# Performance work log

Hardware: AMD Instinct MI355X
Metric: run time of the kernel (lower is better)

## Reference

```python
import jax, jax.numpy as jnp
import numpy as np
from jax import lax

DIM = 180
NH = 6
WS = (16, 16)          # window_size
BWS = (8, 8)           # base_win_size (min of base and window)
HEAD_DIM = DIM // (2 * NH)      # 15
SCALE = HEAD_DIM
POS_DIM = (DIM // 4) // 4       # 11 (DynamicPosBias pos_dim on dim//4)
B, H, W = 2, 256, 256
L = WS[0] * WS[1]               # 256 tokens per window
ML = BWS[0] * BWS[1]            # 64 downsampled tokens
R = L // ML                     # 4, spatial_linear in_features


def _rel_index():
    Hs, Ws = WS
    coords = np.stack(np.meshgrid(np.arange(Hs), np.arange(Ws), indexing='ij')).reshape(2, -1)
    rel = (coords[:, :, None] - coords[:, None, :]).transpose(1, 2, 0)
    rel[..., 0] += Hs - 1
    rel[..., 1] += Ws - 1
    rel[..., 0] *= 2 * Ws - 1
    return jnp.asarray(rel.sum(-1).reshape(-1))  # (L*L,) indices into (2H-1)*(2W-1)


def _bias_grid():
    Hs, Ws = WS
    g = np.stack(np.meshgrid(np.arange(1 - Hs, Hs), np.arange(1 - Ws, Ws), indexing='ij'))
    return jnp.asarray(g.reshape(2, -1).T.astype(np.float32))  # ((2H-1)*(2W-1), 2)

REL_IDX = _rel_index()
BIAS_GRID = _bias_grid()


def _ln(x, g, b):
    m = x.mean(-1, keepdims=True)
    v = ((x - m) ** 2).mean(-1, keepdims=True)
    return (x - m) / jnp.sqrt(v + 1e-5) * g + b


def window_partition(x, ws):
    Bn, Hn, Wn, C = x.shape
    x = x.reshape(Bn, Hn // ws[0], ws[0], Wn // ws[1], ws[1], C)
    return x.transpose(0, 1, 3, 2, 4, 5).reshape(-1, ws[0], ws[1], C)


def window_reverse(w, ws, Hn, Wn):
    Bn = w.shape[0] * (ws[0] * ws[1]) // (Hn * Wn)
    x = w.reshape(Bn, Hn // ws[0], Wn // ws[1], ws[0], ws[1], -1)
    return x.transpose(0, 1, 3, 2, 4, 5).reshape(Bn, Hn, Wn, -1)


def setup_inputs():
    key = jax.random.key(0)
    ks = jax.random.split(key, 16)
    s = 0.02
    rn = lambda k, shape: jax.random.normal(k, shape, jnp.float32) * s
    C5 = DIM // 5
    return {
        'x': jax.random.normal(ks[0], (B, H, W, DIM), jnp.float32),
        'conv1_w': rn(ks[1], (DIM, C5)), 'conv1_b': jnp.zeros((C5,), jnp.float32),
        'conv2_w': rn(ks[2], (3, 3, C5, C5)), 'conv2_b': jnp.zeros((C5,), jnp.float32),
        'conv3_w': rn(ks[3], (C5, DIM)), 'conv3_b': jnp.zeros((DIM,), jnp.float32),
        'dfe_lin_w': rn(ks[4], (DIM, DIM)), 'dfe_lin_b': jnp.zeros((DIM,), jnp.float32),
        'sl_w': rn(ks[5], (R,)), 'sl_b': jnp.zeros((), jnp.float32),
        'pos_proj_w': rn(ks[6], (2, POS_DIM)), 'pos_proj_b': jnp.zeros((POS_DIM,), jnp.float32),
        'ln1_g': jnp.ones((POS_DIM,), jnp.float32), 'ln1_b': jnp.zeros((POS_DIM,), jnp.float32),
        'mlp1_w': rn(ks[7], (POS_DIM, POS_DIM)), 'mlp1_b': jnp.zeros((POS_DIM,), jnp.float32),
        'ln2_g': jnp.ones((POS_DIM,), jnp.float32), 'ln2_b': jnp.zeros((POS_DIM,), jnp.float32),
        'mlp2_w': rn(ks[8], (POS_DIM, POS_DIM)), 'mlp2_b': jnp.zeros((POS_DIM,), jnp.float32),
        'ln3_g': jnp.ones((POS_DIM,), jnp.float32), 'ln3_b': jnp.zeros((POS_DIM,), jnp.float32),
        'mlp3_w': rn(ks[9], (POS_DIM, NH)), 'mlp3_b': jnp.zeros((NH,), jnp.float32),
        'proj_w': rn(ks[10], (DIM, DIM)), 'proj_b': jnp.zeros((DIM,), jnp.float32),
    }


def reference(x, conv1_w, conv1_b, conv2_w, conv2_b, conv3_w, conv3_b,
              dfe_lin_w, dfe_lin_b, sl_w, sl_b, pos_proj_w, pos_proj_b,
              ln1_g, ln1_b, mlp1_w, mlp1_b, ln2_g, ln2_b, mlp2_w, mlp2_b,
              ln3_g, ln3_b, mlp3_w, mlp3_b, proj_w, proj_b):
    xB, xH, xW, xC = x.shape

    # ---- DFE: qv = conv(x) * linear(x), both in NHWC ----
    y = jax.nn.leaky_relu(x @ conv1_w + conv1_b, 0.2)
    y = lax.conv_general_dilated(y, conv2_w, (1, 1), 'SAME',
                                 dimension_numbers=('NHWC', 'HWIO', 'NHWC'))
    y = jax.nn.leaky_relu(y + conv2_b, 0.2)
    y = y @ conv3_w + conv3_b
    qv = y * (x @ dfe_lin_w + dfe_lin_b)            # (B,H,W,C)

    # ---- window partition + q/v head split ----
    qv = window_partition(qv, WS).reshape(-1, L, xC)       # (Bw,L,C)
    Bw = qv.shape[0]
    qv = qv.reshape(Bw, L, 2, NH, HEAD_DIM).transpose(2, 0, 3, 1, 4)
    q, v = qv[0], qv[1]                                    # (Bw,NH,L,hd)

    # ---- spatial self-correlation ----
    mH, mW = BWS
    rH, rW = WS[0] // mH, WS[1] // mW
    v_ = v.reshape(Bw, NH, mH, rH, mW, rW, HEAD_DIM)
    v_ = v_.transpose(0, 1, 2, 4, 6, 3, 5).reshape(Bw, NH, ML, HEAD_DIM, rH * rW)
    vp = jnp.einsum('bhmcr,r->bhmc', v_, sl_w) + sl_b      # (Bw,NH,ML,hd)

    corr = jnp.einsum('bhlc,bhmc->bhlm', q, vp) / SCALE    # (Bw,NH,L,ML)

    # dynamic relative position bias MLP (residual=False)
    p = BIAS_GRID @ pos_proj_w + pos_proj_b
    p = jax.nn.relu(_ln(p, ln1_g, ln1_b)) @ mlp1_w + mlp1_b
    p = jax.nn.relu(_ln(p, ln2_g, ln2_b)) @ mlp2_w + mlp2_b
    p = jax.nn.relu(_ln(p, ln3_g, ln3_b)) @ mlp3_w + mlp3_b  # ((2H-1)*(2W-1), NH)

    rpb = p[REL_IDX].reshape(L, mH, rH, mW, rW, NH)
    rpb = rpb.transpose(0, 1, 3, 5, 2, 4).reshape(L, ML, NH, rH * rW).mean(-1)
    rpb = rpb.transpose(2, 0, 1)                            # (NH,L,ML)
    corr = corr + rpb[None]

    x_sp = jnp.einsum('bhlm,bhmc->bhlc', corr, vp)
    x_sp = x_sp.transpose(0, 2, 1, 3).reshape(Bw, L, NH * HEAD_DIM)

    # ---- channel self-correlation ----
    qc = q.transpose(0, 2, 1, 3).reshape(Bw, L, NH * HEAD_DIM)
    vc = v.transpose(0, 2, 1, 3).reshape(Bw, L, NH * HEAD_DIM)
    cc = jnp.einsum('blc,bld->bcd', qc, vc) / L
    x_ch = jnp.einsum('bcd,bld->blc', cc, vc)

    # ---- merge windows, concat, project ----
    half = xC // 2
    x_sp = window_reverse(x_sp.reshape(-1, WS[0], WS[1], half), WS, xH, xW)
    x_ch = window_reverse(x_ch.reshape(-1, WS[0], WS[1], half), WS, xH, xW)
    out = jnp.concatenate([x_sp, x_ch], -1) @ proj_w + proj_b
    return out
```

## Files before the change

kernel.cpp:

```cpp
#include <hip/hip_runtime.h>
#include <hip/hip_fp16.h>

typedef unsigned int uint32;
typedef _Float16 f16;
typedef f16 f16x4 __attribute__((ext_vector_type(4)));
typedef f16 f16x8 __attribute__((ext_vector_type(8)));
typedef float f32x4 __attribute__((ext_vector_type(4)));

union U8 { f16x8 v; uint4 u4; uint2 u2[2]; f16 h[8]; };

__device__ __forceinline__ float h2f(__half v) { return __half2float(v); }
__device__ __forceinline__ __half f2h(float v) { return __float2half(v); }

__global__ __launch_bounds__(256) void k0_w1(const float* __restrict__ W1,
                                             f16* __restrict__ W1T) {
  int i = blockIdx.x * 256 + threadIdx.x;
  if (i < 9216) {
    int n = i / 192, k = i % 192;
    W1T[i] = (n < 36 && k < 180) ? (f16)W1[k * 36 + n] : (f16)0;
  }
}

__global__ __launch_bounds__(256) void k1_conv1(const float* __restrict__ X,
                                                const f16* __restrict__ W1T,
                                                const float* __restrict__ B1,
                                                __half* __restrict__ T1) {
  int t = threadIdx.x;
  int p0 = blockIdx.x * 128;
  int lane = t & 63, wave = t >> 6;
  int lm = lane & 15, lq = lane >> 4;

  f16x8 ax[6][2];
#pragma unroll
  for (int mt = 0; mt < 2; ++mt) {
    int row = p0 + wave * 32 + mt * 16 + lm;
    const float* xr = X + (size_t)row * 180;
#pragma unroll
    for (int ch = 0; ch < 6; ++ch) {
      int k0 = ch * 32 + lq * 8;
      U8 v; v.u4 = (uint4){0u, 0u, 0u, 0u};
      if (k0 + 8 <= 180) {
        float4 a = *(const float4*)&xr[k0];
        float4 b = *(const float4*)&xr[k0 + 4];
        v.h[0]=(f16)a.x; v.h[1]=(f16)a.y; v.h[2]=(f16)a.z; v.h[3]=(f16)a.w;
        v.h[4]=(f16)b.x; v.h[5]=(f16)b.y; v.h[6]=(f16)b.z; v.h[7]=(f16)b.w;
      } else if (k0 < 180) {
        float4 a = *(const float4*)&xr[k0];
        v.h[0]=(f16)a.x; v.h[1]=(f16)a.y; v.h[2]=(f16)a.z; v.h[3]=(f16)a.w;
      }
      ax[ch][mt] = v.v;
    }
  }

  f32x4 acc[2][3];
#pragma unroll
  for (int mt = 0; mt < 2; ++mt)
#pragma unroll
    for (int nt = 0; nt < 3; ++nt) acc[mt][nt] = (f32x4){0.f, 0.f, 0.f, 0.f};

#pragma unroll
  for (int ch = 0; ch < 6; ++ch) {
#pragma unroll
    for (int nt = 0; nt < 3; ++nt) {
      int n = nt * 16 + lm;
      f16x8 bf = *(const f16x8*)&W1T[n * 192 + ch * 32 + lq * 8];
      acc[0][nt] = __builtin_amdgcn_mfma_f32_16x16x32_f16(
          ax[ch][0], bf, acc[0][nt], 0, 0, 0);
      acc[1][nt] = __builtin_amdgcn_mfma_f32_16x16x32_f16(
          ax[ch][1], bf, acc[1][nt], 0, 0, 0);
    }
  }

  float bb[3];
#pragma unroll
  for (int nt = 0; nt < 3; ++nt) {
    int co = nt * 16 + lm;
    bb[nt] = (co < 36) ? B1[co] : 0.f;
  }
#pragma unroll
  for (int mt = 0; mt < 2; ++mt) {
#pragma unroll
    for (int reg = 0; reg < 4; ++reg) {
      int p = p0 + wave * 32 + mt * 16 + lq * 4 + reg;
      __half* o = T1 + (size_t)p * 36;
#pragma unroll
      for (int nt = 0; nt < 3; ++nt) {
        int co = nt * 16 + lm;
        if (co < 36) {
          float v = acc[mt][nt][reg] + bb[nt];
          o[co] = f2h(v > 0.f ? v : 0.2f * v);
        }
      }
    }
  }
}

__global__ __launch_bounds__(256) void k0_w2(const float* __restrict__ W2,
                                             f16* __restrict__ W2T) {
  int i = blockIdx.x * 256 + threadIdx.x;
  if (i < 17280) {
    int tap = i / 1920, rem = i % 1920, n = rem / 40, k = rem % 40;
    W2T[i] = (n < 36 && k < 36) ? (f16)W2[(tap * 36 + k) * 36 + n] : (f16)0;
  }
}

__global__ __launch_bounds__(256) void k2_conv2(const __half* __restrict__ T1,
                                                const f16* __restrict__ W2T,
                                                const float* __restrict__ B2,
                                                __half* __restrict__ T2) {
  __shared__ __align__(16) f16 ins[3 * 132 * 40];
  int t = threadIdx.x;
  int p0 = blockIdx.x * 128;
  int b = p0 >> 16, y = (p0 >> 8) & 255, x0 = p0 & 255;

  const uint32* T1u = (const uint32*)T1;
  uint32* insu = (uint32*)ins;
  for (int i = t; i < 7920; i += 256) {
    int kh = i / 2640, rem = i % 2640;
    int xx = rem / 20, u = rem % 20;
    int ry = y + kh - 1, gx = x0 + xx - 1;
    uint32 v = 0u;
    if (u < 18 && xx < 130 && (unsigned)ry < 256u && (unsigned)gx < 256u)
      v = T1u[((size_t)((b * 256 + ry) * 256 + gx)) * 18 + u];
    insu[i] = v;
  }
  __syncthreads();

  int lane = t & 63, wave = t >> 6;
  int lm = lane & 15, lq = lane >> 4;
  const f16x8 zero8 = {(f16)0,(f16)0,(f16)0,(f16)0,(f16)0,(f16)0,(f16)0,(f16)0};

  f32x4 acc[2][3];
#pragma unroll
  for (int mt = 0; mt < 2; ++mt)
#pragma unroll
    for (int nt = 0; nt < 3; ++nt) acc[mt][nt] = (f32x4){0.f, 0.f, 0.f, 0.f};

#pragma unroll
  for (int kh = 0; kh < 3; ++kh) {
#pragma unroll
    for (int kw = 0; kw < 3; ++kw) {
      int tap = kh * 3 + kw;
      f16x8 a0[2], a1[2];
#pragma unroll
      for (int mt = 0; mt < 2; ++mt) {
        int xx = wave * 32 + mt * 16 + lm + kw;
        const f16* ar = &ins[(kh * 132 + xx) * 40];
        a0[mt] = *(const f16x8*)&ar[lq * 8];
        a1[mt] = (lq == 0) ? *(const f16x8*)&ar[32] : zero8;
      }
#pragma unroll
      for (int nt = 0; nt < 3; ++nt) {
        const f16* br = &W2T[(tap * 48 + nt * 16 + lm) * 40];
        f16x8 b0 = *(const f16x8*)&br[lq * 8];
        f16x8 b1 = (lq == 0) ? *(const f16x8*)&br[32] : zero8;
#pragma unroll
        for (int mt = 0; mt < 2; ++mt) {
          acc[mt][nt] = __builtin_amdgcn_mfma_f32_16x16x32_f16(
              a0[mt], b0, acc[mt][nt], 0, 0, 0);
          acc[mt][nt] = __builtin_amdgcn_mfma_f32_16x16x32_f16(
              a1[mt], b1, acc[mt][nt], 0, 0, 0);
        }
      }
    }
  }

  float bb[3];
#pragma unroll
  for (int nt = 0; nt < 3; ++nt) {
    int co = nt * 16 + lm;
    bb[nt] = (co < 36) ? B2[co] : 0.f;
  }
#pragma unroll
  for (int mt = 0; mt < 2; ++mt) {
#pragma unroll
    for (int reg = 0; reg < 4; ++reg) {
      int p = p0 + wave * 32 + mt * 16 + lq * 4 + reg;
      __half* o = T2 + (size_t)p * 36;
#pragma unroll
      for (int nt = 0; nt < 3; ++nt) {
        int co = nt * 16 + lm;
        if (co < 36) {
          float v = acc[mt][nt][reg] + bb[nt];
          o[co] = f2h(v > 0.f ? v : 0.2f * v);
        }
      }
    }
  }
}

__global__ __launch_bounds__(256) void k0_wt(const float* __restrict__ SW3,
                                             const float* __restrict__ SWD,
                                             f16* __restrict__ WT3,
                                             f16* __restrict__ WTD) {
  int tid = blockIdx.x * 256 + threadIdx.x;
  int stride = gridDim.x * 256;
  for (int i = tid; i < 192 * 40; i += stride) {
    int n = i / 40, k = i % 40;
    WT3[i] = (n < 180 && k < 36) ? (f16)SW3[k * 180 + n] : (f16)0;
  }
  for (int i = tid; i < 192 * 192; i += stride) {
    int n = i / 192, k = i % 192;
    WTD[i] = (n < 180 && k < 180) ? (f16)SWD[k * 180 + n] : (f16)0;
  }
}

__global__ __launch_bounds__(256) void k0_pw(const float* __restrict__ SPW,
                                             f16* __restrict__ PWT) {
  int tid = blockIdx.x * 256 + threadIdx.x;
  int stride = gridDim.x * 256;
  for (int i = tid; i < 192 * 192; i += stride) {
    int n = i / 192, k = i % 192;
    PWT[i] = (n < 180 && k < 180) ? (f16)SPW[k * 180 + n] : (f16)0;
  }
}

__global__ __launch_bounds__(256) void k3_qv(const float* __restrict__ X,
                                             const __half* __restrict__ T2,
                                             const f16* __restrict__ WT3,
                                             const f16* __restrict__ WTD,
                                             const float* __restrict__ B3,
                                             const float* __restrict__ BD,
                                             __half* __restrict__ QX) {
  __shared__ __align__(16) f16 eplds[4 * 32 * 56];
  int t = threadIdx.x;
  int p0 = blockIdx.x * 128;
  int lane = t & 63, wave = t >> 6;
  int lm = lane & 15, lq = lane >> 4;

  const f16x8 zero8 = {(f16)0,(f16)0,(f16)0,(f16)0,(f16)0,(f16)0,(f16)0,(f16)0};

  f16x8 ax[6][2];
  f16x8 at0[2];
  f16x8 at1[2];
#pragma unroll
  for (int mt = 0; mt < 2; ++mt) {
    int row = p0 + wave * 32 + mt * 16 + lm;
    const float* xr = X + (size_t)row * 180;
#pragma unroll
    for (int ch = 0; ch < 6; ++ch) {
      int k0 = ch * 32 + lq * 8;
      U8 v; v.u4 = (uint4){0u, 0u, 0u, 0u};
      if (k0 + 8 <= 180) {
        float4 a = *(const float4*)&xr[k0];
        float4 b = *(const float4*)&xr[k0 + 4];
        v.h[0]=(f16)a.x; v.h[1]=(f16)a.y; v.h[2]=(f16)a.z; v.h[3]=(f16)a.w;
        v.h[4]=(f16)b.x; v.h[5]=(f16)b.y; v.h[6]=(f16)b.z; v.h[7]=(f16)b.w;
      } else if (k0 < 180) {
        float4 a = *(const float4*)&xr[k0];
        v.h[0]=(f16)a.x; v.h[1]=(f16)a.y; v.h[2]=(f16)a.z; v.h[3]=(f16)a.w;
      }
      ax[ch][mt] = v.v;
    }
    const f16* tr = (const f16*)T2 + (size_t)row * 36;
    U8 tv;
    tv.u2[0] = *(const uint2*)&tr[lq * 8];
    tv.u2[1] = *(const uint2*)&tr[lq * 8 + 4];
    at0[mt] = tv.v;
    U8 t1v; t1v.u4 = (uint4){0u, 0u, 0u, 0u};
    if (lq == 0) t1v.u2[0] = *(const uint2*)&tr[32];
    at1[mt] = t1v.v;
  }

  f16* myl = eplds + wave * 1792;
  for (int bn = 0; bn < 4; ++bn) {
    int n0 = bn * 48;
    f32x4 accC[2][3], accD[2][3];
#pragma unroll
    for (int i = 0; i < 2; ++i)
#pragma unroll
      for (int j = 0; j < 3; ++j) {
        accC[i][j] = (f32x4){0.f, 0.f, 0.f, 0.f};
        accD[i][j] = (f32x4){0.f, 0.f, 0.f, 0.f};
      }

#pragma unroll
    for (int nt = 0; nt < 3; ++nt) {
      int n = n0 + nt * 16 + lm;
      f16x8 b0 = *(const f16x8*)&WT3[n * 40 + lq * 8];
      f16x8 b1 = (lq == 0) ? *(const f16x8*)&WT3[n * 40 + 32] : zero8;
#pragma unroll
      for (int mt = 0; mt < 2; ++mt) {
        accC[mt][nt] = __builtin_amdgcn_mfma_f32_16x16x32_f16(
            at0[mt], b0, accC[mt][nt], 0, 0, 0);
        accC[mt][nt] = __builtin_amdgcn_mfma_f32_16x16x32_f16(
            at1[mt], b1, accC[mt][nt], 0, 0, 0);
      }
    }

#pragma unroll
    for (int ch = 0; ch < 6; ++ch) {
#pragma unroll
      for (int nt = 0; nt < 3; ++nt) {
        int n = n0 + nt * 16 + lm;
        f16x8 bf = *(const f16x8*)&WTD[n * 192 + ch * 32 + lq * 8];
        accD[0][nt] = __builtin_amdgcn_mfma_f32_16x16x32_f16(
            ax[ch][0], bf, accD[0][nt], 0, 0, 0);
        accD[1][nt] = __builtin_amdgcn_mfma_f32_16x16x32_f16(
            ax[ch][1], bf, accD[1][nt], 0, 0, 0);
      }
    }

    float cb[3], db[3];
#pragma unroll
    for (int nt = 0; nt < 3; ++nt) {
      int col = n0 + nt * 16 + lm;
      cb[nt] = (col < 180) ? B3[col] : 0.f;
      db[nt] = (col < 180) ? BD[col] : 0.f;
    }
#pragma unroll
    for (int mt = 0; mt < 2; ++mt)
#pragma unroll
      for (int reg = 0; reg < 4; ++reg) {
        int r = mt * 16 + lq * 4 + reg;
#pragma unroll
        for (int nt = 0; nt < 3; ++nt)
          myl[r * 56 + nt * 16 + lm] =
              (f16)((accC[mt][nt][reg] + cb[nt]) *
                    (accD[mt][nt][reg] + db[nt]) * 64.f);
      }
#pragma unroll
    for (int it = 0; it < 6; ++it) {
      int idx = it * 64 + lane;
      int r = idx / 12, c4 = idx % 12;
      int col = n0 + c4 * 4;
      if (col < 180) {
        int p = p0 + wave * 32 + r;
        int b = p >> 16, y = (p >> 8) & 255, x = p & 255;
        int wi = (b << 8) | ((y >> 4) << 4) | (x >> 4);
        int l = ((y & 15) << 4) | (x & 15);
        uint2 val = *(const uint2*)&myl[r * 56 + c4 * 4];
        *(uint2*)((f16*)QX + ((size_t)(wi * 256 + l)) * 180 + col) = val;
      }
    }
  }
}

__device__ __forceinline__ void ln_relu11(const float* p, const float* g,
                                          const float* b, float* r) {
  float m = 0.f;
#pragma unroll
  for (int j = 0; j < 11; ++j) m += p[j];
  m *= (1.0f / 11.0f);
  float v = 0.f;
#pragma unroll
  for (int j = 0; j < 11; ++j) { float d = p[j] - m; v += d * d; }
  v *= (1.0f / 11.0f);
  float inv = 1.0f / sqrtf(v + 1e-5f);
#pragma unroll
  for (int j = 0; j < 11; ++j) {
    float xn = (p[j] - m) * inv * g[j] + b[j];
    r[j] = fmaxf(xn, 0.f);
  }
}
__device__ __forceinline__ void mm11(const float* r, const float* W,
                                     const float* b, float* o) {
#pragma unroll
  for (int j2 = 0; j2 < 11; ++j2) {
    float s = b[j2];
#pragma unroll
    for (int j = 0; j < 11; ++j) s += r[j] * W[j * 11 + j2];
    o[j2] = s;
  }
}

__global__ __launch_bounds__(256) void k5a_posmlp(
    const float* PPW, const float* PPB,
    const float* LN1G, const float* LN1B, const float* M1W, const float* M1B,
    const float* LN2G, const float* LN2B, const float* M2W, const float* M2B,
    const float* LN3G, const float* LN3B, const float* M3W, const float* M3B,
    float* __restrict__ PTAB) {
  int t = blockIdx.x * 256 + threadIdx.x;
  if (t >= 961) return;
  float g0 = (float)(t / 31) - 15.0f;
  float g1 = (float)(t % 31) - 15.0f;
  float p[11], r[11];
#pragma unroll
  for (int j = 0; j < 11; ++j)
    p[j] = g0 * PPW[j] + g1 * PPW[11 + j] + PPB[j];
  ln_relu11(p, LN1G, LN1B, r);
  mm11(r, M1W, M1B, p);
  ln_relu11(p, LN2G, LN2B, r);
  mm11(r, M2W, M2B, p);
  ln_relu11(p, LN3G, LN3B, r);
#pragma unroll
  for (int h = 0; h < 6; ++h) {
    float s = M3B[h];
#pragma unroll
    for (int j = 0; j < 11; ++j) s += r[j] * M3W[j * 6 + h];
    PTAB[t * 6 + h] = s;
  }
}

__global__ __launch_bounds__(256) void k5b_rpb(const float* __restrict__ PTAB,
                                               float* __restrict__ RPB) {
  int t = blockIdx.x * 256 + threadIdx.x;
  int m = t & 63;
  int l = (t >> 6) & 255;
  int h = t >> 14;
  int mh = m >> 3, mw = m & 7;
  int qr = l >> 4, qc = l & 15;
  float s = 0.f;
#pragma unroll
  for (int rh = 0; rh < 2; ++rh)
#pragma unroll
    for (int rw = 0; rw < 2; ++rw) {
      int dr = qr - (mh * 2 + rh) + 15;
      int dc = qc - (mw * 2 + rw) + 15;
      s += PTAB[(dr * 31 + dc) * 6 + h];
    }
  RPB[t] = 0.25f * s;
}

__global__ __launch_bounds__(256) void k7a_cc(const __half* __restrict__ QX,
                                              float* __restrict__ CC) {
  __shared__ __half qs[64 * 90];
  __shared__ __half vs[64 * 90];
  int wi = blockIdx.x, t = threadIdx.x;
  int c0 = (t % 15) * 6, d0 = (t / 15) * 6;
  bool act = t < 225;
  float acc[36];
#pragma unroll
  for (int i = 0; i < 36; ++i) acc[i] = 0.f;
  const uint32* G = (const uint32*)(QX + (size_t)wi * 46080);
  uint32* qsw = (uint32*)qs;
  uint32* vsw = (uint32*)vs;
  for (int pass = 0; pass < 4; ++pass) {
    __syncthreads();
    for (int i = t; i < 2880; i += 256) {
      int l = i / 45, k = i % 45;
      int gw = (pass * 64 + l) * 90;
      qsw[l * 45 + k] = G[gw + k];
      vsw[l * 45 + k] = G[gw + 45 + k];
    }
    __syncthreads();
    if (act) {
      for (int l = 0; l < 64; ++l) {
        const __half2* qh = (const __half2*)&qs[l * 90 + c0];
        const __half2* vh = (const __half2*)&vs[l * 90 + d0];
        float a[6], b[6];
#pragma unroll
        for (int k = 0; k < 3; ++k) {
          __half2 x = qh[k];
          a[2 * k] = __low2float(x); a[2 * k + 1] = __high2float(x);
          __half2 y = vh[k];
          b[2 * k] = __low2float(y); b[2 * k + 1] = __high2float(y);
        }
#pragma unroll
        for (int i = 0; i < 6; ++i)
#pragma unroll
          for (int j = 0; j < 6; ++j) acc[i * 6 + j] += a[i] * b[j];
      }
    }
  }
  if (act) {
    const float s = 1.0f / (256.0f * 4096.0f);
#pragma unroll
    for (int i = 0; i < 6; ++i)
#pragma unroll
      for (int j = 0; j < 6; ++j)
        CC[((size_t)(wi * 90 + c0 + i)) * 90 + d0 + j] = acc[i * 6 + j] * s;
  }
}

__global__ __launch_bounds__(256) void kA_xsp(__half* __restrict__ QX,
                                              const float* __restrict__ RPB,
                                              const float* __restrict__ SLW,
                                              const float* __restrict__ SLB) {
  __shared__ __align__(16) unsigned char SM[80384];
  f16* U   = (f16*)SM;
  f16* vpS = (f16*)(SM + 53248);
  f16* vpT = (f16*)(SM + 66560);
  int wi = blockIdx.x, t = threadIdx.x;
  __half* QW = QX + (size_t)wi * 46080;
  const uint32* G = (const uint32*)QW;
  uint32* Uw = (uint32*)U;

  for (int i = t; i < 11520; i += 256) {
    int l = i / 45, k = i % 45;
    Uw[l * 45 + k] = G[l * 90 + 45 + k];
  }
  __syncthreads();
  float w0 = SLW[0], w1 = SLW[1], w2 = SLW[2], w3 = SLW[3];
  float sb = SLB[0];
  for (int e = t; e < 6144; e += 256) {
    int m = e & 63, idx = e >> 6;
    int c = idx & 15, h = idx >> 4;
    f16 val = (f16)0;
    if (c < 15) {
      int ch = h * 15 + c;
      int lb = (m >> 3) * 32 + (m & 7) * 2;
      float s = w0 * (float)U[lb * 90 + ch] + w1 * (float)U[(lb + 1) * 90 + ch]
              + w2 * (float)U[(lb + 16) * 90 + ch] + w3 * (float)U[(lb + 17) * 90 + ch];
      val = (f16)(s * 4.f + sb * 256.f);
    }
    vpS[m * 104 + idx] = val;
    vpT[idx * 72 + m] = val;
  }
  __syncthreads();
  for (int j = t; j < 1536; j += 256) {
    int h = j >> 8, l = j & 255;
    U[l * 104 + h * 16 + 15] = (f16)0;
  }
  for (int i = t; i < 11520; i += 256) {
    int l = i / 45, k = i % 45;
    union { uint32 w; f16 h[2]; } cv;
    cv.w = G[l * 90 + k];
    int cg0 = 2 * k, cg1 = 2 * k + 1;
    int h0 = cg0 / 15, c0 = cg0 - h0 * 15;
    int h1 = cg1 / 15, c1 = cg1 - h1 * 15;
    U[l * 104 + h0 * 16 + c0] = cv.h[0];
    U[l * 104 + h1 * 16 + c1] = cv.h[1];
  }
  __syncthreads();

  int lane = t & 63, w = t >> 6;
  int lm = lane & 15, lq = lane >> 4;
  const float invA = 1.0f / 960.0f;
  for (int h = 0; h < 6; ++h) {
    f16x4 a1[4], b1[4];
#pragma unroll
    for (int mt = 0; mt < 4; ++mt)
      a1[mt] = *(const f16x4*)&vpS[(mt * 16 + lm) * 104 + h * 16 + lq * 4];
#pragma unroll
    for (int lt = 0; lt < 4; ++lt)
      b1[lt] = *(const f16x4*)&U[(w * 64 + lt * 16 + lm) * 104 + h * 16 + lq * 4];
    f32x4 acc1[4][4];
#pragma unroll
    for (int mt = 0; mt < 4; ++mt)
#pragma unroll
      for (int lt = 0; lt < 4; ++lt)
        acc1[mt][lt] = __builtin_amdgcn_mfma_f32_16x16x16f16(
            a1[mt], b1[lt], (f32x4){0.f, 0.f, 0.f, 0.f}, 0, 0, 0);
    f16x4 b2[4][4];
#pragma unroll
    for (int lt = 0; lt < 4; ++lt) {
      int l = w * 64 + lt * 16 + lm;
      const float* rp = RPB + ((size_t)(h * 256 + l)) * 64;
#pragma unroll
      for (int mt = 0; mt < 4; ++mt) {
        float4 rv = *(const float4*)&rp[mt * 16 + lq * 4];
        f16x4 bb;
        bb[0] = (f16)(acc1[mt][lt][0] * invA + rv.x * 256.f);
        bb[1] = (f16)(acc1[mt][lt][1] * invA + rv.y * 256.f);
        bb[2] = (f16)(acc1[mt][lt][2] * invA + rv.z * 256.f);
        bb[3] = (f16)(acc1[mt][lt][3] * invA + rv.w * 256.f);
        b2[mt][lt] = bb;
      }
    }
    f16x4 a2[4];
#pragma unroll
    for (int kt = 0; kt < 4; ++kt)
      a2[kt] = *(const f16x4*)&vpT[(h * 16 + lm) * 72 + kt * 16 + lq * 4];
#pragma unroll
    for (int lt = 0; lt < 4; ++lt) {
      f32x4 acc2 = (f32x4){0.f, 0.f, 0.f, 0.f};
#pragma unroll
      for (int kt = 0; kt < 4; ++kt)
        acc2 = __builtin_amdgcn_mfma_f32_16x16x16f16(a2[kt], b2[kt][lt], acc2, 0, 0, 0);
      int l = w * 64 + lt * 16 + lm;
      __half* orow = QW + l * 180 + h * 15;
#pragma unroll
      for (int reg = 0; reg < 4; ++reg) {
        int c = lq * 4 + reg;
        if (c < 15) orow[c] = f2h(acc2[reg] * 0.125f);
      }
    }
  }
}

__global__ __launch_bounds__(256) void kB_xch(__half* __restrict__ QX,
                                              const float* __restrict__ CC) {
  __shared__ __align__(16) f16 vA[256 * 104];
  __shared__ __align__(16) f16 ccB[96 * 104];
  int wi = blockIdx.x, t = threadIdx.x;
  __half* QW = QX + (size_t)wi * 46080;
  const uint32* G = (const uint32*)QW;
  uint32* vAw = (uint32*)vA;
  for (int i = t; i < 12288; i += 256) {
    int l = i / 48, kk = i % 48;
    vAw[l * 52 + kk] = (kk < 45) ? G[l * 90 + 45 + kk] : 0u;
  }
  const float* ccg = CC + (size_t)wi * 8100;
  uint32* ccw = (uint32*)ccB;
  for (int i = t; i < 4992; i += 256) {
    int c = i / 52, dd = i % 52;
    uint32 out = 0u;
    if (c < 90 && dd < 45) {
      float2 f = *(const float2*)&ccg[c * 90 + dd * 2];
      union { uint32 w; f16 h[2]; } cv;
      cv.h[0] = (f16)(f.x * 65536.f);
      cv.h[1] = (f16)(f.y * 65536.f);
      out = cv.w;
    }
    ccw[c * 52 + dd] = out;
  }
  __syncthreads();
  int lane = t & 63, w = t >> 6;
  int lm = lane & 15, lq = lane >> 4;
  f32x4 acc[4][6];
#pragma unroll
  for (int mt = 0; mt < 4; ++mt)
#pragma unroll
    for (int nt = 0; nt < 6; ++nt) acc[mt][nt] = (f32x4){0.f, 0.f, 0.f, 0.f};
  for (int kc = 0; kc < 3; ++kc) {
    f16x8 af[4], bf[6];
#pragma unroll
    for (int mt = 0; mt < 4; ++mt)
      af[mt] = *(const f16x8*)&vA[(w * 64 + mt * 16 + lm) * 104 + kc * 32 + lq * 8];
#pragma unroll
    for (int nt = 0; nt < 6; ++nt)
      bf[nt] = *(const f16x8*)&ccB[(nt * 16 + lm) * 104 + kc * 32 + lq * 8];
#pragma unroll
    for (int mt = 0; mt < 4; ++mt)
#pragma unroll
      for (int nt = 0; nt < 6; ++nt)
        acc[mt][nt] = __builtin_amdgcn_mfma_f32_16x16x32_f16(
            af[mt], bf[nt], acc[mt][nt], 0, 0, 0);
  }
#pragma unroll
  for (int mt = 0; mt < 4; ++mt) {
#pragma unroll
    for (int reg = 0; reg < 4; ++reg) {
      int l = w * 64 + mt * 16 + lq * 4 + reg;
      __half* orow = QW + l * 180 + 90;
#pragma unroll
      for (int nt = 0; nt < 6; ++nt) {
        int c = nt * 16 + lm;
        if (c < 90) orow[c] = f2h(acc[mt][nt][reg] * 0.001953125f);
      }
    }
  }
}

__global__ __launch_bounds__(256) void k8_proj(const __half* __restrict__ XS,
                                               const f16* __restrict__ PWT,
                                               const float* __restrict__ PB,
                                               float* __restrict__ OUT) {
  int t = threadIdx.x;
  int w0r = blockIdx.x * 128;
  int lane = t & 63, wave = t >> 6;
  int lm = lane & 15, lq = lane >> 4;

  f16x8 ax[6][2];
#pragma unroll
  for (int mt = 0; mt < 2; ++mt) {
    int row = w0r + wave * 32 + mt * 16 + lm;
    const f16* xr = (const f16*)XS + (size_t)row * 180;
#pragma unroll
    for (int ch = 0; ch < 6; ++ch) {
      int k0 = ch * 32 + lq * 8;
      U8 v; v.u4 = (uint4){0u, 0u, 0u, 0u};
      if (k0 + 8 <= 180) {
        v.u2[0] = *(const uint2*)&xr[k0];
        v.u2[1] = *(const uint2*)&xr[k0 + 4];
      } else if (k0 < 180) {
        v.u2[0] = *(const uint2*)&xr[k0];
      }
      ax[ch][mt] = v.v;
    }
  }

  for (int bn = 0; bn < 4; ++bn) {
    int n0 = bn * 48;
    f32x4 acc[2][3];
#pragma unroll
    for (int i = 0; i < 2; ++i)
#pragma unroll
      for (int j = 0; j < 3; ++j) acc[i][j] = (f32x4){0.f, 0.f, 0.f, 0.f};

#pragma unroll
    for (int ch = 0; ch < 6; ++ch) {
#pragma unroll
      for (int nt = 0; nt < 3; ++nt) {
        int n = n0 + nt * 16 + lm;
        f16x8 bf = *(const f16x8*)&PWT[n * 192 + ch * 32 + lq * 8];
        acc[0][nt] = __builtin_amdgcn_mfma_f32_16x16x32_f16(
            ax[ch][0], bf, acc[0][nt], 0, 0, 0);
        acc[1][nt] = __builtin_amdgcn_mfma_f32_16x16x32_f16(
            ax[ch][1], bf, acc[1][nt], 0, 0, 0);
      }
    }

    float pb[3];
#pragma unroll
    for (int nt = 0; nt < 3; ++nt) {
      int col = n0 + nt * 16 + lm;
      pb[nt] = (col < 180) ? PB[col] : 0.f;
    }
    const float inv = 1.0f / 8192.0f;
#pragma unroll
    for (int mt = 0; mt < 2; ++mt) {
#pragma unroll
      for (int reg = 0; reg < 4; ++reg) {
        int w = w0r + wave * 32 + mt * 16 + lq * 4 + reg;
        int wi = w >> 8, l = w & 255;
        int b = wi >> 8, wy = (wi >> 4) & 15, wx = wi & 15;
        int ly = l >> 4, lx = l & 15;
        int p = (b << 16) | (((wy << 4) | ly) << 8) | ((wx << 4) | lx);
        float* orow = OUT + (size_t)p * 180;
#pragma unroll
        for (int nt = 0; nt < 3; ++nt) {
          int col = n0 + nt * 16 + lm;
          if (col < 180) orow[col] = acc[mt][nt][reg] * inv + pb[nt];
        }
      }
    }
  }
}

extern "C" void kernel_launch(void* const* d_in, const int* in_sizes, int n_in,
                              void* d_out, int out_size, void* d_ws, size_t ws_size,
                              hipStream_t stream) {
  const float* X    = (const float*)d_in[0];
  const float* W1   = (const float*)d_in[1];
  const float* B1   = (const float*)d_in[2];
  const float* W2   = (const float*)d_in[3];
  const float* B2   = (const float*)d_in[4];
  const float* W3   = (const float*)d_in[5];
  const float* B3c  = (const float*)d_in[6];
  const float* WD   = (const float*)d_in[7];
  const float* BD   = (const float*)d_in[8];
  const float* SLW  = (const float*)d_in[9];
  const float* SLB  = (const float*)d_in[10];
  const float* PPW  = (const float*)d_in[11];
  const float* PPB  = (const float*)d_in[12];
  const float* LN1G = (const float*)d_in[13];
  const float* LN1B = (const float*)d_in[14];
  const float* M1W  = (const float*)d_in[15];
  const float* M1B  = (const float*)d_in[16];
  const float* LN2G = (const float*)d_in[17];
  const float* LN2B = (const float*)d_in[18];
  const float* M2W  = (const float*)d_in[19];
  const float* M2B  = (const float*)d_in[20];
  const float* LN3G = (const float*)d_in[21];
  const float* LN3B = (const float*)d_in[22];
  const float* M3W  = (const float*)d_in[23];
  const float* M3B  = (const float*)d_in[24];
  const float* PW   = (const float*)d_in[25];
  const float* PB   = (const float*)d_in[26];
  float* OUT = (float*)d_out;

  char* ws = (char*)d_ws;
  f16*   W2T  = (f16*)(ws);
  f16*   W1T  = (f16*)(ws + 34560);
  __half* QX  = (__half*)(ws);
  __half* T1  = (__half*)(ws + 47185920);
  __half* T2  = (__half*)(ws + 56623104);
  float* PTAB = (float*)(ws + 47185920);
  float* RPB  = (float*)(ws + 47212544);
  f16*   WT3  = (f16*)(ws + 47605760);
  f16*   WTD  = (f16*)(ws + 47621120);
  float* CC   = (float*)(ws + 47605760);
  f16*   PWT  = (f16*)(ws + 64194560);

  hipLaunchKernelGGL(k0_w2, dim3(68), dim3(256), 0, stream, W2, W2T);
  hipLaunchKernelGGL(k0_w1, dim3(36), dim3(256), 0, stream, W1, W1T);
  hipLaunchKernelGGL(k1_conv1, dim3(1024), dim3(256), 0, stream, X, W1T, B1, T1);
  hipLaunchKernelGGL(k2_conv2, dim3(1024), dim3(256), 0, stream, T1, W2T, B2, T2);
  hipLaunchKernelGGL(k0_wt, dim3(144), dim3(256), 0, stream, W3, WD, WT3, WTD);
  hipLaunchKernelGGL(k3_qv, dim3(1024), dim3(256), 0, stream, X, T2, WT3, WTD, B3c, BD, QX);
  hipLaunchKernelGGL(k0_pw, dim3(144), dim3(256), 0, stream, PW, PWT);
  hipLaunchKernelGGL(k5a_posmlp, dim3(4), dim3(256), 0, stream,
                     PPW, PPB, LN1G, LN1B, M1W, M1B, LN2G, LN2B, M2W, M2B,
                     LN3G, LN3B, M3W, M3B, PTAB);
  hipLaunchKernelGGL(k5b_rpb, dim3(384), dim3(256), 0, stream, PTAB, RPB);
  hipLaunchKernelGGL(k7a_cc, dim3(512), dim3(256), 0, stream, QX, CC);
  hipLaunchKernelGGL(kA_xsp, dim3(512), dim3(256), 0, stream, QX, RPB, SLW, SLB);
  hipLaunchKernelGGL(kB_xch, dim3(512), dim3(256), 0, stream, QX, CC);
  hipLaunchKernelGGL(k8_proj, dim3(1024), dim3(256), 0, stream, QX, PWT, PB, OUT);
}
```

Baseline: 525.6 us.

## Fuse channel-correlation, spatial attention and channel output into one per-window kernel

Replaces three per-window kernels (cc computation, spatial correlation, channel output) with a single kernel that loads each window's q and v into LDS once. The channel-correlation matrix now stays in LDS as fp16 instead of making a round-trip through a global fp32 buffer, and two launches disappear. In exchange the kernel uses about 150 KB of LDS, which limits it to one block per CU. Its phases then run back to back with barriers between them, with less latency hiding.

```diff
diff --git a/kernel.cpp b/kernel.cpp
--- a/kernel.cpp
+++ b/kernel.cpp
@@ -412,32 +412,45 @@
   RPB[t] = 0.25f * s;
 }
 
-__global__ __launch_bounds__(256) void k7a_cc(const __half* __restrict__ QX,
-                                              float* __restrict__ CC) {
-  __shared__ __half qs[64 * 90];
-  __shared__ __half vs[64 * 90];
+__global__ __launch_bounds__(256) void kW_win(__half* __restrict__ QX,
+                                              const float* __restrict__ RPB,
+                                              const float* __restrict__ SLW,
+                                              const float* __restrict__ SLB) {
+  __shared__ __align__(16) unsigned char SMW[153600];
+  f16* vA  = (f16*)SMW;
+  f16* QU  = (f16*)(SMW + 53248);
+  f16* vpS = (f16*)(SMW + 106496);
+  f16* vpT = (f16*)(SMW + 119808);
+  f16* ccs = (f16*)(SMW + 133632);
   int wi = blockIdx.x, t = threadIdx.x;
-  int c0 = (t % 15) * 6, d0 = (t / 15) * 6;
-  bool act = t < 225;
-  float acc[36];
-#pragma unroll
-  for (int i = 0; i < 36; ++i) acc[i] = 0.f;
-  const uint32* G = (const uint32*)(QX + (size_t)wi * 46080);
-  uint32* qsw = (uint32*)qs;
-  uint32* vsw = (uint32*)vs;
-  for (int pass = 0; pass < 4; ++pass) {
-    __syncthreads();
-    for (int i = t; i < 2880; i += 256) {
-      int l = i / 45, k = i % 45;
-      int gw = (pass * 64 + l) * 90;
-      qsw[l * 45 + k] = G[gw + k];
-      vsw[l * 45 + k] = G[gw + 45 + k];
-    }
-    __syncthreads();
-    if (act) {
-      for (int l = 0; l < 64; ++l) {
-        const __half2* qh = (const __half2*)&qs[l * 90 + c0];
-        const __half2* vh = (const __half2*)&vs[l * 90 + d0];
+  __half* QW = QX + (size_t)wi * 46080;
+  const uint32* G = (const uint32*)QW;
+
+  uint32* vAw = (uint32*)vA;
+  for (int i = t; i < 12288; i += 256) {
+    int l = i / 48, kk = i % 48;
+    vAw[l * 52 + kk] = (kk < 45) ? G[l * 90 + 45 + kk] : 0u;
+  }
+  uint32* qlw = (uint32*)QU;
+  for (int i = t; i < 11520; i += 256) {
+    int l = i / 45, k = i % 45;
+    qlw[l * 45 + k] = G[l * 90 + k];
+  }
+  for (int i = t; i < 9984; i += 256) {
+    int c = i / 104, d = i % 104;
+    if (c >= 90 || d >= 90) ccs[i] = (f16)0;
+  }
+  __syncthreads();
+
+  {
+    int c0 = (t % 15) * 6, d0 = (t / 15) * 6;
+    if (t < 225) {
+      float acc[36];
+#pragma unroll
+      for (int i = 0; i < 36; ++i) acc[i] = 0.f;
+      for (int l = 0; l < 256; ++l) {
+        const __half2* qh = (const __half2*)&QU[l * 90 + c0];
+        const __half2* vh = (const __half2*)&vA[l * 104 + d0];
         float a[6], b[6];
 #pragma unroll
         for (int k = 0; k < 3; ++k) {
@@ -451,183 +464,139 @@
 #pragma unroll
           for (int j = 0; j < 6; ++j) acc[i * 6 + j] += a[i] * b[j];
       }
-    }
-  }
-  if (act) {
-    const float s = 1.0f / (256.0f * 4096.0f);
-#pragma unroll
-    for (int i = 0; i < 6; ++i)
-#pragma unroll
-      for (int j = 0; j < 6; ++j)
-        CC[((size_t)(wi * 90 + c0 + i)) * 90 + d0 + j] = acc[i * 6 + j] * s;
-  }
-}
-
-__global__ __launch_bounds__(256) void kA_xsp(__half* __restrict__ QX,
-                                              const float* __restrict__ RPB,
-                                              const float* __restrict__ SLW,
-                                              const float* __restrict__ SLB) {
-  __shared__ __align__(16) unsigned char SM[80384];
-  f16* U   = (f16*)SM;
-  f16* vpS = (f16*)(SM + 53248);
-  f16* vpT = (f16*)(SM + 66560);
-  int wi = blockIdx.x, t = threadIdx.x;
-  __half* QW = QX + (size_t)wi * 46080;
-  const uint32* G = (const uint32*)QW;
-  uint32* Uw = (uint32*)U;
-
-  for (int i = t; i < 11520; i += 256) {
-    int l = i / 45, k = i % 45;
-    Uw[l * 45 + k] = G[l * 90 + 45 + k];
+#pragma unroll
+      for (int i = 0; i < 6; ++i)
+#pragma unroll
+        for (int j = 0; j < 6; ++j)
+          ccs[(c0 + i) * 104 + d0 + j] = (f16)(acc[i * 6 + j] * 0.0625f);
+    }
   }
   __syncthreads();
-  float w0 = SLW[0], w1 = SLW[1], w2 = SLW[2], w3 = SLW[3];
-  float sb = SLB[0];
-  for (int e = t; e < 6144; e += 256) {
-    int m = e & 63, idx = e >> 6;
-    int c = idx & 15, h = idx >> 4;
-    f16 val = (f16)0;
-    if (c < 15) {
-      int ch = h * 15 + c;
-      int lb = (m >> 3) * 32 + (m & 7) * 2;
-      float s = w0 * (float)U[lb * 90 + ch] + w1 * (float)U[(lb + 1) * 90 + ch]
-              + w2 * (float)U[(lb + 16) * 90 + ch] + w3 * (float)U[(lb + 17) * 90 + ch];
-      val = (f16)(s * 4.f + sb * 256.f);
-    }
-    vpS[m * 104 + idx] = val;
-    vpT[idx * 72 + m] = val;
-  }
-  __syncthreads();
-  for (int j = t; j < 1536; j += 256) {
-    int h = j >> 8, l = j & 255;
-    U[l * 104 + h * 16 + 15] = (f16)0;
-  }
-  for (int i = t; i < 11520; i += 256) {
-    int l = i / 45, k = i % 45;
-    union { uint32 w; f16 h[2]; } cv;
-    cv.w = G[l * 90 + k];
-    int cg0 = 2 * k, cg1 = 2 * k + 1;
-    int h0 = cg0 / 15, c0 = cg0 - h0 * 15;
-    int h1 = cg1 / 15, c1 = cg1 - h1 * 15;
-    U[l * 104 + h0 * 16 + c0] = cv.h[0];
-    U[l * 104 + h1 * 16 + c1] = cv.h[1];
+
+  {
+    float w0 = SLW[0], w1 = SLW[1], w2 = SLW[2], w3 = SLW[3];
+    float sb = SLB[0];
+    for (int e = t; e < 6144; e += 256) {
+      int m = e & 63, idx = e >> 6;
+      int c = idx & 15, h = idx >> 4;
+      f16 val = (f16)0;
+      if (c < 15) {
+        int ch = h * 15 + c;
+        int lb = (m >> 3) * 32 + (m & 7) * 2;
+        float s = w0 * (float)vA[lb * 104 + ch] + w1 * (float)vA[(lb + 1) * 104 + ch]
+                + w2 * (float)vA[(lb + 16) * 104 + ch] + w3 * (float)vA[(lb + 17) * 104 + ch];
+        val = (f16)(s * 4.f + sb * 256.f);
+      }
+      vpS[m * 104 + idx] = val;
+      vpT[idx * 72 + m] = val;
+    }
+    for (int j = t; j < 1536; j += 256) {
+      int h = j >> 8, l = j & 255;
+      QU[l * 104 + h * 16 + 15] = (f16)0;
+    }
+    for (int i = t; i < 11520; i += 256) {
+      int l = i / 45, k = i % 45;
+      union { uint32 w; f16 h[2]; } cv;
+      cv.w = G[l * 90 + k];
+      int cg0 = 2 * k, cg1 = 2 * k + 1;
+      int h0 = cg0 / 15, c0 = cg0 - h0 * 15;
+      int h1 = cg1 / 15, c1 = cg1 - h1 * 15;
+      QU[l * 104 + h0 * 16 + c0] = cv.h[0];
+      QU[l * 104 + h1 * 16 + c1] = cv.h[1];
+    }
   }
   __syncthreads();
 
   int lane = t & 63, w = t >> 6;
   int lm = lane & 15, lq = lane >> 4;
-  const float invA = 1.0f / 960.0f;
-  for (int h = 0; h < 6; ++h) {
-    f16x4 a1[4], b1[4];
+
+  {
+    const float invA = 1.0f / 960.0f;
+    for (int h = 0; h < 6; ++h) {
+      f16x4 a1[4], b1[4];
+#pragma unroll
+      for (int mt = 0; mt < 4; ++mt)
+        a1[mt] = *(const f16x4*)&vpS[(mt * 16 + lm) * 104 + h * 16 + lq * 4];
+#pragma unroll
+      for (int lt = 0; lt < 4; ++lt)
+        b1[lt] = *(const f16x4*)&QU[(w * 64 + lt * 16 + lm) * 104 + h * 16 + lq * 4];
+      f32x4 acc1[4][4];
+#pragma unroll
+      for (int mt = 0; mt < 4; ++mt)
+#pragma unroll
+        for (int lt = 0; lt < 4; ++lt)
+          acc1[mt][lt] = __builtin_amdgcn_mfma_f32_16x16x16f16(
+              a1[mt], b1[lt], (f32x4){0.f, 0.f, 0.f, 0.f}, 0, 0, 0);
+      f16x4 b2[4][4];
+#pragma unroll
+      for (int lt = 0; lt < 4; ++lt) {
+        int l = w * 64 + lt * 16 + lm;
+        const float* rp = RPB + ((size_t)(h * 256 + l)) * 64;
+#pragma unroll
+        for (int mt = 0; mt < 4; ++mt) {
+          float4 rv = *(const float4*)&rp[mt * 16 + lq * 4];
+          f16x4 bb;
+          bb[0] = (f16)(acc1[mt][lt][0] * invA + rv.x * 256.f);
+          bb[1] = (f16)(acc1[mt][lt][1] * invA + rv.y * 256.f);
+          bb[2] = (f16)(acc1[mt][lt][2] * invA + rv.z * 256.f);
+          bb[3] = (f16)(acc1[mt][lt][3] * invA + rv.w * 256.f);
+          b2[mt][lt] = bb;
+        }
+      }
+      f16x4 a2[4];
+#pragma unroll
+      for (int kt = 0; kt < 4; ++kt)
+        a2[kt] = *(const f16x4*)&vpT[(h * 16 + lm) * 72 + kt * 16 + lq * 4];
+#pragma unroll
+      for (int lt = 0; lt < 4; ++lt) {
+        f32x4 acc2 = (f32x4){0.f, 0.f, 0.f, 0.f};
+#pragma unroll
+        for (int kt = 0; kt < 4; ++kt)
+          acc2 = __builtin_amdgcn_mfma_f32_16x16x16f16(a2[kt], b2[kt][lt], acc2, 0, 0, 0);
+        int l = w * 64 + lt * 16 + lm;
+        __half* orow = QW + l * 180 + h * 15;
+#pragma unroll
+        for (int reg = 0; reg < 4; ++reg) {
+          int c = lq * 4 + reg;
+          if (c < 15) orow[c] = f2h(acc2[reg] * 0.125f);
+        }
+      }
+    }
+  }
+  __syncthreads();
+
+  {
+    f32x4 acc[4][6];
 #pragma unroll
     for (int mt = 0; mt < 4; ++mt)
-      a1[mt] = *(const f16x4*)&vpS[(mt * 16 + lm) * 104 + h * 16 + lq * 4];
-#pragma unroll
-    for (int lt = 0; lt < 4; ++lt)
-      b1[lt] = *(const f16x4*)&U[(w * 64 + lt * 16 + lm) * 104 + h * 16 + lq * 4];
-    f32x4 acc1[4][4];
-#pragma unroll
-    for (int mt = 0; mt < 4; ++mt)
-#pragma unroll
-      for (int lt = 0; lt < 4; ++lt)
-        acc1[mt][lt] = __builtin_amdgcn_mfma_f32_16x16x16f16(
-            a1[mt], b1[lt], (f32x4){0.f, 0.f, 0.f, 0.f}, 0, 0, 0);
-    f16x4 b2[4][4];
-#pragma unroll
-    for (int lt = 0; lt < 4; ++lt) {
-      int l = w * 64 + lt * 16 + lm;
-      const float* rp = RPB + ((size_t)(h * 256 + l)) * 64;
-#pragma unroll
-      for (int mt = 0; mt < 4; ++mt) {
-        float4 rv = *(const float4*)&rp[mt * 16 + lq * 4];
-        f16x4 bb;
-        bb[0] = (f16)(acc1[mt][lt][0] * invA + rv.x * 256.f);
-        bb[1] = (f16)(acc1[mt][lt][1] * invA + rv.y * 256.f);
-        bb[2] = (f16)(acc1[mt][lt][2] * invA + rv.z * 256.f);
-        bb[3] = (f16)(acc1[mt][lt][3] * invA + rv.w * 256.f);
-        b2[mt][lt] = bb;
-      }
-    }
-    f16x4 a2[4];
-#pragma unroll
-    for (int kt = 0; kt < 4; ++kt)
-      a2[kt] = *(const f16x4*)&vpT[(h * 16 + lm) * 72 + kt * 16 + lq * 4];
-#pragma unroll
-    for (int lt = 0; lt < 4; ++lt) {
-      f32x4 acc2 = (f32x4){0.f, 0.f, 0.f, 0.f};
-#pragma unroll
-      for (int kt = 0; kt < 4; ++kt)
-        acc2 = __builtin_amdgcn_mfma_f32_16x16x16f16(a2[kt], b2[kt][lt], acc2, 0, 0, 0);
-      int l = w * 64 + lt * 16 + lm;
-      __half* orow = QW + l * 180 + h * 15;
+#pragma unroll
+      for (int nt = 0; nt < 6; ++nt) acc[mt][nt] = (f32x4){0.f, 0.f, 0.f, 0.f};
+    for (int kc = 0; kc < 3; ++kc) {
+      f16x8 af[4], bf[6];
+#pragma unroll
+      for (int mt = 0; mt < 4; ++mt)
+        af[mt] = *(const f16x8*)&vA[(w * 64 + mt * 16 + lm) * 104 + kc * 32 + lq * 8];
+#pragma unroll
+      for (int nt = 0; nt < 6; ++nt)
+        bf[nt] = *(const f16x8*)&ccs[(nt * 16 + lm) * 104 + kc * 32 + lq * 8];
+#pragma unroll
+      for (int mt = 0; mt < 4; ++mt)
+#pragma unroll
+        for (int nt = 0; nt < 6; ++nt)
+          acc[mt][nt] = __builtin_amdgcn_mfma_f32_16x16x32_f16(
+              af[mt], bf[nt], acc[mt][nt], 0, 0, 0);
+    }
+#pragma unroll
+    for (int mt = 0; mt < 4; ++mt) {
 #pragma unroll
       for (int reg = 0; reg < 4; ++reg) {
-        int c = lq * 4 + reg;
-        if (c < 15) orow[c] = f2h(acc2[reg] * 0.125f);
-      }
-    }
-  }
-}
-
-__global__ __launch_bounds__(256) void kB_xch(__half* __restrict__ QX,
-                                              const float* __restrict__ CC) {
-  __shared__ __align__(16) f16 vA[256 * 104];
-  __shared__ __align__(16) f16 ccB[96 * 104];
-  int wi = blockIdx.x, t = threadIdx.x;
-  __half* QW = QX + (size_t)wi * 46080;
-  const uint32* G = (const uint32*)QW;
-  uint32* vAw = (uint32*)vA;
-  for (int i = t; i < 12288; i += 256) {
-    int l = i / 48, kk = i % 48;
-    vAw[l * 52 + kk] = (kk < 45) ? G[l * 90 + 45 + kk] : 0u;
-  }
-  const float* ccg = CC + (size_t)wi * 8100;
-  uint32* ccw = (uint32*)ccB;
-  for (int i = t; i < 4992; i += 256) {
-    int c = i / 52, dd = i % 52;
-    uint32 out = 0u;
-    if (c < 90 && dd < 45) {
-      float2 f = *(const float2*)&ccg[c * 90 + dd * 2];
-      union { uint32 w; f16 h[2]; } cv;
-      cv.h[0] = (f16)(f.x * 65536.f);
-      cv.h[1] = (f16)(f.y * 65536.f);
-      out = cv.w;
-    }
-    ccw[c * 52 + dd] = out;
-  }
-  __syncthreads();
-  int lane = t & 63, w = t >> 6;
-  int lm = lane & 15, lq = lane >> 4;
-  f32x4 acc[4][6];
-#pragma unroll
-  for (int mt = 0; mt < 4; ++mt)
-#pragma unroll
-    for (int nt = 0; nt < 6; ++nt) acc[mt][nt] = (f32x4){0.f, 0.f, 0.f, 0.f};
-  for (int kc = 0; kc < 3; ++kc) {
-    f16x8 af[4], bf[6];
-#pragma unroll
-    for (int mt = 0; mt < 4; ++mt)
-      af[mt] = *(const f16x8*)&vA[(w * 64 + mt * 16 + lm) * 104 + kc * 32 + lq * 8];
-#pragma unroll
-    for (int nt = 0; nt < 6; ++nt)
-      bf[nt] = *(const f16x8*)&ccB[(nt * 16 + lm) * 104 + kc * 32 + lq * 8];
-#pragma unroll
-    for (int mt = 0; mt < 4; ++mt)
-#pragma unroll
-      for (int nt = 0; nt < 6; ++nt)
-        acc[mt][nt] = __builtin_amdgcn_mfma_f32_16x16x32_f16(
-            af[mt], bf[nt], acc[mt][nt], 0, 0, 0);
-  }
-#pragma unroll
-  for (int mt = 0; mt < 4; ++mt) {
-#pragma unroll
-    for (int reg = 0; reg < 4; ++reg) {
-      int l = w * 64 + mt * 16 + lq * 4 + reg;
-      __half* orow = QW + l * 180 + 90;
-#pragma unroll
-      for (int nt = 0; nt < 6; ++nt) {
-        int c = nt * 16 + lm;
-        if (c < 90) orow[c] = f2h(acc[mt][nt][reg] * 0.001953125f);
+        int l = w * 64 + mt * 16 + lq * 4 + reg;
+        __half* orow = QW + l * 180 + 90;
+#pragma unroll
+        for (int nt = 0; nt < 6; ++nt) {
+          int c = nt * 16 + lm;
+          if (c < 90) orow[c] = f2h(acc[mt][nt][reg] * 0.001953125f);
+        }
       }
     }
   }
@@ -751,7 +720,6 @@
   float* RPB  = (float*)(ws + 47212544);
   f16*   WT3  = (f16*)(ws + 47605760);
   f16*   WTD  = (f16*)(ws + 47621120);
-  float* CC   = (float*)(ws + 47605760);
   f16*   PWT  = (f16*)(ws + 64194560);
 
   hipLaunchKernelGGL(k0_w2, dim3(68), dim3(256), 0, stream, W2, W2T);
@@ -765,8 +733,6 @@
                      PPW, PPB, LN1G, LN1B, M1W, M1B, LN2G, LN2B, M2W, M2B,
                      LN3G, LN3B, M3W, M3B, PTAB);
   hipLaunchKernelGGL(k5b_rpb, dim3(384), dim3(256), 0, stream, PTAB, RPB);
-  hipLaunchKernelGGL(k7a_cc, dim3(512), dim3(256), 0, stream, QX, CC);
-  hipLaunchKernelGGL(kA_xsp, dim3(512), dim3(256), 0, stream, QX, RPB, SLW, SLB);
-  hipLaunchKernelGGL(kB_xch, dim3(512), dim3(256), 0, stream, QX, CC);
+  hipLaunchKernelGGL(kW_win, dim3(512), dim3(256), 0, stream, QX, RPB, SLW, SLB);
   hipLaunchKernelGGL(k8_proj, dim3(1024), dim3(256), 0, stream, QX, PWT, PB, OUT);
 }
```

Result: no change. 526.7 us (+0.2%).
